# Optimization experiments

Hardware: AMD Instinct MI355X
Metric: run time of the kernel (lower is better)

## Reference

```python
import jax, jax.numpy as jnp
import numpy as np

B, M, N, D = 32, 10, 1000, 128
DEMAND_SCALER, SPEED_SCALER, PREF_SCALER = 40.0, 1.0, 1.0


def _pos_encoding(m, d, dtype):
    # standard sinusoidal PE over agent positions 0..m-1
    pos = jnp.arange(m, dtype=dtype)[:, None]
    div = jnp.exp(jnp.arange(0, d, 2, dtype=dtype) * (-jnp.log(jnp.asarray(10000.0, dtype)) / d))
    ang = pos * div  # (m, d/2)
    return jnp.stack([jnp.sin(ang), jnp.cos(ang)], axis=-1).reshape(m, d)  # even=sin, odd=cos


def setup_inputs() -> dict:
    key = jax.random.key(0)
    ks = jax.random.split(key, 14)
    return {
        "locs": jax.random.uniform(ks[0], (B, M + N, 2), jnp.float32),
        "capacity": jax.random.uniform(ks[1], (B, M), jnp.float32),
        "speed": jax.random.uniform(ks[2], (B, M), jnp.float32),
        "demand": jax.random.uniform(ks[3], (B, 1, M + N), jnp.float32),
        "agents_preference": jax.random.uniform(ks[4], (B, M, M + N), jnp.float32),
        "action_mask": jnp.ones((B, M, M + N), dtype=bool),
        "W_depot": jax.random.normal(ks[5], (D, 2), jnp.float32) * 0.1,
        "W_posproj": jax.random.normal(ks[6], (D, D), jnp.float32) * 0.05,
        "alpha": jnp.ones((1,), jnp.float32),
        "W_agents": jax.random.normal(ks[7], (D, 4), jnp.float32) * 0.1,
        "W_depot_agents": jax.random.normal(ks[8], (D, 2 * D), jnp.float32) * 0.05,
        "W_clients": jax.random.normal(ks[9], (D, 5), jnp.float32) * 0.1,
        "W_pref": jax.random.normal(ks[10], (D, 1), jnp.float32) * 0.1,
        "W_final": jax.random.normal(ks[11], (D, 3 * D), jnp.float32) * 0.05,
    }


def reference(locs, capacity, speed, demand, agents_preference, action_mask,
              W_depot, W_posproj, alpha, W_agents, W_depot_agents, W_clients,
              W_pref, W_final):
    m = action_mask.shape[-2]
    d = W_final.shape[0]
    depot_locs = locs[:, :m]            # (B, m, 2)
    agents_locs = locs[:, :m]
    clients_locs = locs[:, m:]          # (B, N, 2)

    # depot branch with positional encoding
    dep_emb = depot_locs @ W_depot.T                                   # (B, m, D)
    pe = _pos_encoding(m, d, dep_emb.dtype)                            # (m, D)
    depot_embedding = dep_emb + alpha[0] * (pe @ W_posproj.T)          # broadcast over B

    # agents branch
    agents_feats = jnp.concatenate(
        [agents_locs, capacity[..., None] / DEMAND_SCALER, speed[..., None] / SPEED_SCALER], axis=-1)
    agents_embedding = agents_feats @ W_agents.T                       # (B, m, D)
    depot_agents_embedding = jnp.concatenate(
        [depot_embedding, agents_embedding], axis=-1) @ W_depot_agents.T  # (B, m, D)

    # clients branch (with polar feats)
    demands = demand[:, 0, m:]                                         # (B, N)
    centered = clients_locs - depot_locs[:, 0:1]                       # (B, N, 2)
    dist = jnp.linalg.norm(centered, axis=-1, keepdims=True)
    angle = jnp.arctan2(centered[..., 1:], centered[..., :1])
    clients_feats = jnp.concatenate(
        [clients_locs, demands[..., None] / DEMAND_SCALER, dist, angle], axis=-1)
    clients_embedding = clients_feats @ W_clients.T                    # (B, N, D)

    nodes_embedding = jnp.concatenate([agents_embedding, clients_embedding], axis=1)  # (B, m+N, D)

    # fused final projection: Linear(3D, D) on cat([nodes, pref_embed, depot_agents])
    # == nodes @ Wn.T  +  pref_embed @ Wp.T  +  depot_agents @ Wd.T, broadcast over dims.
    # pref_embed = pref[..., None] * W_pref[:, 0]  (rank-1), so pref_embed @ Wp.T = pref[..., None] * (Wp @ W_pref[:, 0])
    Wn, Wp, Wd = W_final[:, :d], W_final[:, d:2 * d], W_final[:, 2 * d:]
    v_pref = Wp @ W_pref[:, 0]                                         # (D,)
    pref = agents_preference / PREF_SCALER                             # (B, m, m+N)
    combined_embedding = (
        (nodes_embedding @ Wn.T)[:, None, :, :]                        # (B, 1, m+N, D)
        + pref[..., None] * v_pref                                     # (B, m, m+N, D)
        + (depot_agents_embedding @ Wd.T)[:, :, None, :]               # (B, m, 1, D)
    )
    return nodes_embedding, combined_embedding
```

## Files before the change

### kernel.cpp

```cpp
#include <hip/hip_runtime.h>
#include <math.h>

#define BB 32
#define MM 10
#define NNODES 1010
#define DD 128
#define RPB 16
#define NG ((NNODES + RPB - 1) / RPB)

__global__ __launch_bounds__(DD) void k_agents(
    const float* __restrict__ locs,
    const float* __restrict__ capacity,
    const float* __restrict__ speed,
    const float* __restrict__ W_depot,
    const float* __restrict__ W_posproj,
    const float* __restrict__ alpha,
    const float* __restrict__ W_agents,
    const float* __restrict__ W_da,
    const float* __restrict__ W_pref,
    const float* __restrict__ W_final,
    float* __restrict__ out_nodes,
    float* __restrict__ ws_daWd,
    float* __restrict__ ws_vpref)
{
    const int b = blockIdx.x / MM;
    const int m = blockIdx.x % MM;
    const int d = threadIdx.x;

    __shared__ float pe_s[DD];
    __shared__ float dep_s[DD];
    __shared__ float ag_s[DD];
    __shared__ float da_s[DD];

    {
        const int i = d >> 1;
        const float div = expf((float)(2 * i) * (-logf(10000.0f) / (float)DD));
        const float ang = (float)m * div;
        pe_s[d] = (d & 1) ? cosf(ang) : sinf(ang);
    }
    __syncthreads();

    float pp = 0.0f;
    {
        const float4* wp = (const float4*)(W_posproj + (size_t)d * DD);
        #pragma unroll 4
        for (int k4 = 0; k4 < DD / 4; ++k4) {
            float4 w = wp[k4];
            const float* p = &pe_s[k4 * 4];
            pp = fmaf(w.x, p[0], pp);
            pp = fmaf(w.y, p[1], pp);
            pp = fmaf(w.z, p[2], pp);
            pp = fmaf(w.w, p[3], pp);
        }
    }

    const float lx = locs[((size_t)b * NNODES + m) * 2 + 0];
    const float ly = locs[((size_t)b * NNODES + m) * 2 + 1];
    const float dep = fmaf(lx, W_depot[d * 2 + 0],
                      fmaf(ly, W_depot[d * 2 + 1], alpha[0] * pp));

    const float cap = capacity[b * MM + m] * (1.0f / 40.0f);
    const float spd = speed[b * MM + m];
    const float ag = fmaf(lx, W_agents[d * 4 + 0],
                     fmaf(ly, W_agents[d * 4 + 1],
                     fmaf(cap, W_agents[d * 4 + 2],
                          spd * W_agents[d * 4 + 3])));

    out_nodes[((size_t)b * NNODES + m) * DD + d] = ag;

    dep_s[d] = dep;
    ag_s[d] = ag;
    __syncthreads();

    float da = 0.0f;
    {
        const float4* wda = (const float4*)(W_da + (size_t)d * 2 * DD);
        #pragma unroll 4
        for (int k4 = 0; k4 < DD / 4; ++k4) {
            float4 w = wda[k4];
            const float* p = &dep_s[k4 * 4];
            da = fmaf(w.x, p[0], da);
            da = fmaf(w.y, p[1], da);
            da = fmaf(w.z, p[2], da);
            da = fmaf(w.w, p[3], da);
        }
        #pragma unroll 4
        for (int k4 = 0; k4 < DD / 4; ++k4) {
            float4 w = wda[DD / 4 + k4];
            const float* p = &ag_s[k4 * 4];
            da = fmaf(w.x, p[0], da);
            da = fmaf(w.y, p[1], da);
            da = fmaf(w.z, p[2], da);
            da = fmaf(w.w, p[3], da);
        }
    }
    da_s[d] = da;
    __syncthreads();

    float dw = 0.0f;
    {
        const float4* wfd = (const float4*)(W_final + (size_t)d * 3 * DD + 2 * DD);
        #pragma unroll 4
        for (int k4 = 0; k4 < DD / 4; ++k4) {
            float4 w = wfd[k4];
            const float* p = &da_s[k4 * 4];
            dw = fmaf(w.x, p[0], dw);
            dw = fmaf(w.y, p[1], dw);
            dw = fmaf(w.z, p[2], dw);
            dw = fmaf(w.w, p[3], dw);
        }
    }
    ws_daWd[(b * MM + m) * DD + d] = dw;

    if (blockIdx.x == 0) {
        float vp = 0.0f;
        const float4* wfp = (const float4*)(W_final + (size_t)d * 3 * DD + DD);
        const float4* prf = (const float4*)W_pref;
        #pragma unroll 4
        for (int k4 = 0; k4 < DD / 4; ++k4) {
            float4 w = wfp[k4];
            float4 p = prf[k4];
            vp = fmaf(w.x, p.x, vp);
            vp = fmaf(w.y, p.y, vp);
            vp = fmaf(w.z, p.z, vp);
            vp = fmaf(w.w, p.w, vp);
        }
        ws_vpref[d] = vp;
    }
}

__global__ __launch_bounds__(DD) void k_main(
    const float* __restrict__ locs,
    const float* __restrict__ demand,
    const float* __restrict__ pref,
    const float* __restrict__ W_clients,
    const float* __restrict__ W_final,
    const float* __restrict__ ws_daWd,
    const float* __restrict__ ws_vpref,
    float* __restrict__ out_nodes,
    float* __restrict__ out_comb)
{
    const int g = blockIdx.x;
    const int b = blockIdx.y;
    const int tid = threadIdx.x;
    const int n0 = g * RPB;

    __shared__ float rows[RPB][DD];
    __shared__ float feat[RPB][5];

    if (tid < RPB) {
        const int node = n0 + tid;
        if (node < NNODES && node >= MM) {
            const float cx = locs[((size_t)b * NNODES + node) * 2 + 0];
            const float cy = locs[((size_t)b * NNODES + node) * 2 + 1];
            const float d0x = locs[((size_t)b * NNODES + 0) * 2 + 0];
            const float d0y = locs[((size_t)b * NNODES + 0) * 2 + 1];
            const float dx = cx - d0x;
            const float dy = cy - d0y;
            feat[tid][0] = cx;
            feat[tid][1] = cy;
            feat[tid][2] = demand[(size_t)b * NNODES + node] * (1.0f / 40.0f);
            feat[tid][3] = sqrtf(fmaf(dx, dx, dy * dy));
            feat[tid][4] = atan2f(dy, dx);
        }
    }
    __syncthreads();

    {
        const float wc0 = W_clients[tid * 5 + 0];
        const float wc1 = W_clients[tid * 5 + 1];
        const float wc2 = W_clients[tid * 5 + 2];
        const float wc3 = W_clients[tid * 5 + 3];
        const float wc4 = W_clients[tid * 5 + 4];
        #pragma unroll
        for (int r = 0; r < RPB; ++r) {
            const int node = n0 + r;
            float val = 0.0f;
            if (node < NNODES) {
                if (node < MM) {
                    val = out_nodes[((size_t)b * NNODES + node) * DD + tid];
                } else {
                    val = fmaf(feat[r][0], wc0,
                          fmaf(feat[r][1], wc1,
                          fmaf(feat[r][2], wc2,
                          fmaf(feat[r][3], wc3,
                               feat[r][4] * wc4))));
                    out_nodes[((size_t)b * NNODES + node) * DD + tid] = val;
                }
            }
            rows[r][tid] = val;
        }
    }
    __syncthreads();

    const int d = tid;
    float acc[RPB];
    #pragma unroll
    for (int r = 0; r < RPB; ++r) acc[r] = 0.0f;

    {
        const float4* wn = (const float4*)(W_final + (size_t)d * 3 * DD);
        #pragma unroll 4
        for (int k4 = 0; k4 < DD / 4; ++k4) {
            const float4 w = wn[k4];
            #pragma unroll
            for (int r = 0; r < RPB; ++r) {
                const float4 p = *(const float4*)&rows[r][k4 * 4];
                acc[r] = fmaf(w.x, p.x,
                         fmaf(w.y, p.y,
                         fmaf(w.z, p.z,
                         fmaf(w.w, p.w, acc[r]))));
            }
        }
    }

    const float vp = ws_vpref[d];
    float dawd[MM];
    #pragma unroll
    for (int mm = 0; mm < MM; ++mm)
        dawd[mm] = ws_daWd[(b * MM + mm) * DD + d];

    for (int r = 0; r < RPB; ++r) {
        const int node = n0 + r;
        if (node >= NNODES) break;
        #pragma unroll
        for (int mm = 0; mm < MM; ++mm) {
            const float pr = pref[(size_t)(b * MM + mm) * NNODES + node];
            out_comb[((size_t)(b * MM + mm) * NNODES + node) * DD + d] =
                fmaf(pr, vp, acc[r] + dawd[mm]);
        }
    }
}

extern "C" void kernel_launch(void* const* d_in, const int* in_sizes, int n_in,
                              void* d_out, int out_size, void* d_ws, size_t ws_size,
                              hipStream_t stream) {
    const float* locs       = (const float*)d_in[0];
    const float* capacity   = (const float*)d_in[1];
    const float* speed      = (const float*)d_in[2];
    const float* demand     = (const float*)d_in[3];
    const float* agents_pref= (const float*)d_in[4];
    const float* W_depot    = (const float*)d_in[6];
    const float* W_posproj  = (const float*)d_in[7];
    const float* alpha      = (const float*)d_in[8];
    const float* W_agents   = (const float*)d_in[9];
    const float* W_da       = (const float*)d_in[10];
    const float* W_clients  = (const float*)d_in[11];
    const float* W_pref     = (const float*)d_in[12];
    const float* W_final    = (const float*)d_in[13];

    float* out_nodes = (float*)d_out;
    float* out_comb  = out_nodes + (size_t)BB * NNODES * DD;

    float* ws_daWd  = (float*)d_ws;
    float* ws_vpref = ws_daWd + BB * MM * DD;

    k_agents<<<dim3(BB * MM), DD, 0, stream>>>(
        locs, capacity, speed, W_depot, W_posproj, alpha, W_agents,
        W_da, W_pref, W_final, out_nodes, ws_daWd, ws_vpref);

    k_main<<<dim3(NG, BB), DD, 0, stream>>>(
        locs, demand, agents_pref, W_clients, W_final,
        ws_daWd, ws_vpref, out_nodes, out_comb);
}
```

Baseline: 256.8 us.

## Retile main kernel to 4x4 register blocks with float4 stores and split-K agents

The main kernel now handles 32 rows per block with 256 threads. Each thread computes a 4-row by 4-column register tile, which gives weight reuse across rows, and writes the combined output with float4 stores. Preference values are staged in shared memory instead of being read as scattered scalars. The agents kernel uses 512 threads and splits each dot product into four K-partials reduced through shared memory, shortening its serial chains. The output write is bandwidth-bound (about 165MB), so wider stores may help, but fewer blocks and higher register pressure are risks.

```diff
diff --git a/kernel.cpp b/kernel.cpp
--- a/kernel.cpp
+++ b/kernel.cpp
@@ -5,10 +5,10 @@
 #define MM 10
 #define NNODES 1010
 #define DD 128
-#define RPB 16
+#define RPB 32
 #define NG ((NNODES + RPB - 1) / RPB)
 
-__global__ __launch_bounds__(DD) void k_agents(
+__global__ __launch_bounds__(512) void k_agents(
     const float* __restrict__ locs,
     const float* __restrict__ capacity,
     const float* __restrict__ speed,
@@ -25,14 +25,17 @@
 {
     const int b = blockIdx.x / MM;
     const int m = blockIdx.x % MM;
-    const int d = threadIdx.x;
+    const int t = threadIdx.x;
+    const int d = t & (DD - 1);
+    const int q = t >> 7;
 
     __shared__ float pe_s[DD];
     __shared__ float dep_s[DD];
     __shared__ float ag_s[DD];
     __shared__ float da_s[DD];
-
-    {
+    __shared__ float part[4][DD];
+
+    if (q == 0) {
         const int i = d >> 1;
         const float div = expf((float)(2 * i) * (-logf(10000.0f) / (float)DD));
         const float ang = (float)m * div;
@@ -42,94 +45,80 @@
 
     float pp = 0.0f;
     {
-        const float4* wp = (const float4*)(W_posproj + (size_t)d * DD);
-        #pragma unroll 4
-        for (int k4 = 0; k4 < DD / 4; ++k4) {
-            float4 w = wp[k4];
-            const float* p = &pe_s[k4 * 4];
-            pp = fmaf(w.x, p[0], pp);
-            pp = fmaf(w.y, p[1], pp);
-            pp = fmaf(w.z, p[2], pp);
-            pp = fmaf(w.w, p[3], pp);
-        }
-    }
-
-    const float lx = locs[((size_t)b * NNODES + m) * 2 + 0];
-    const float ly = locs[((size_t)b * NNODES + m) * 2 + 1];
-    const float dep = fmaf(lx, W_depot[d * 2 + 0],
-                      fmaf(ly, W_depot[d * 2 + 1], alpha[0] * pp));
-
-    const float cap = capacity[b * MM + m] * (1.0f / 40.0f);
-    const float spd = speed[b * MM + m];
-    const float ag = fmaf(lx, W_agents[d * 4 + 0],
-                     fmaf(ly, W_agents[d * 4 + 1],
-                     fmaf(cap, W_agents[d * 4 + 2],
-                          spd * W_agents[d * 4 + 3])));
-
-    out_nodes[((size_t)b * NNODES + m) * DD + d] = ag;
-
-    dep_s[d] = dep;
-    ag_s[d] = ag;
+        const float4* wp  = (const float4*)(W_posproj + (size_t)d * DD + q * 32);
+        const float4* pe4 = (const float4*)(pe_s + q * 32);
+        #pragma unroll
+        for (int k4 = 0; k4 < 8; ++k4) {
+            const float4 w = wp[k4], p = pe4[k4];
+            pp = fmaf(w.x, p.x, fmaf(w.y, p.y, fmaf(w.z, p.z, fmaf(w.w, p.w, pp))));
+        }
+    }
+    part[q][d] = pp;
+    __syncthreads();
+
+    if (q == 0) {
+        const float ppf = part[0][d] + part[1][d] + part[2][d] + part[3][d];
+        const float lx = locs[((size_t)b * NNODES + m) * 2 + 0];
+        const float ly = locs[((size_t)b * NNODES + m) * 2 + 1];
+        const float dep = fmaf(lx, W_depot[d * 2 + 0],
+                          fmaf(ly, W_depot[d * 2 + 1], alpha[0] * ppf));
+        const float cap = capacity[b * MM + m] * (1.0f / 40.0f);
+        const float spd = speed[b * MM + m];
+        const float ag = fmaf(lx, W_agents[d * 4 + 0],
+                         fmaf(ly, W_agents[d * 4 + 1],
+                         fmaf(cap, W_agents[d * 4 + 2],
+                              spd * W_agents[d * 4 + 3])));
+        out_nodes[((size_t)b * NNODES + m) * DD + d] = ag;
+        dep_s[d] = dep;
+        ag_s[d] = ag;
+    }
     __syncthreads();
 
     float da = 0.0f;
     {
-        const float4* wda = (const float4*)(W_da + (size_t)d * 2 * DD);
-        #pragma unroll 4
-        for (int k4 = 0; k4 < DD / 4; ++k4) {
-            float4 w = wda[k4];
-            const float* p = &dep_s[k4 * 4];
-            da = fmaf(w.x, p[0], da);
-            da = fmaf(w.y, p[1], da);
-            da = fmaf(w.z, p[2], da);
-            da = fmaf(w.w, p[3], da);
-        }
-        #pragma unroll 4
-        for (int k4 = 0; k4 < DD / 4; ++k4) {
-            float4 w = wda[DD / 4 + k4];
-            const float* p = &ag_s[k4 * 4];
-            da = fmaf(w.x, p[0], da);
-            da = fmaf(w.y, p[1], da);
-            da = fmaf(w.z, p[2], da);
-            da = fmaf(w.w, p[3], da);
-        }
-    }
-    da_s[d] = da;
+        const float4* s4  = (const float4*)((q < 2) ? (dep_s + q * 64)
+                                                    : (ag_s + (q - 2) * 64));
+        const float4* wda = (const float4*)(W_da + (size_t)d * 2 * DD + q * 64);
+        #pragma unroll
+        for (int k4 = 0; k4 < 16; ++k4) {
+            const float4 w = wda[k4], p = s4[k4];
+            da = fmaf(w.x, p.x, fmaf(w.y, p.y, fmaf(w.z, p.z, fmaf(w.w, p.w, da))));
+        }
+    }
+    part[q][d] = da;
+    __syncthreads();
+    if (q == 0) da_s[d] = part[0][d] + part[1][d] + part[2][d] + part[3][d];
     __syncthreads();
 
     float dw = 0.0f;
     {
-        const float4* wfd = (const float4*)(W_final + (size_t)d * 3 * DD + 2 * DD);
-        #pragma unroll 4
-        for (int k4 = 0; k4 < DD / 4; ++k4) {
-            float4 w = wfd[k4];
-            const float* p = &da_s[k4 * 4];
-            dw = fmaf(w.x, p[0], dw);
-            dw = fmaf(w.y, p[1], dw);
-            dw = fmaf(w.z, p[2], dw);
-            dw = fmaf(w.w, p[3], dw);
-        }
-    }
-    ws_daWd[(b * MM + m) * DD + d] = dw;
-
-    if (blockIdx.x == 0) {
+        const float4* wfd = (const float4*)(W_final + (size_t)d * 3 * DD + 2 * DD + q * 32);
+        const float4* s4  = (const float4*)(da_s + q * 32);
+        #pragma unroll
+        for (int k4 = 0; k4 < 8; ++k4) {
+            const float4 w = wfd[k4], p = s4[k4];
+            dw = fmaf(w.x, p.x, fmaf(w.y, p.y, fmaf(w.z, p.z, fmaf(w.w, p.w, dw))));
+        }
+    }
+    part[q][d] = dw;
+    __syncthreads();
+    if (q == 0)
+        ws_daWd[(b * MM + m) * DD + d] = part[0][d] + part[1][d] + part[2][d] + part[3][d];
+
+    if (blockIdx.x == 0 && q == 3) {
         float vp = 0.0f;
         const float4* wfp = (const float4*)(W_final + (size_t)d * 3 * DD + DD);
         const float4* prf = (const float4*)W_pref;
-        #pragma unroll 4
+        #pragma unroll
         for (int k4 = 0; k4 < DD / 4; ++k4) {
-            float4 w = wfp[k4];
-            float4 p = prf[k4];
-            vp = fmaf(w.x, p.x, vp);
-            vp = fmaf(w.y, p.y, vp);
-            vp = fmaf(w.z, p.z, vp);
-            vp = fmaf(w.w, p.w, vp);
+            const float4 w = wfp[k4], p = prf[k4];
+            vp = fmaf(w.x, p.x, fmaf(w.y, p.y, fmaf(w.z, p.z, fmaf(w.w, p.w, vp))));
         }
         ws_vpref[d] = vp;
     }
 }
 
-__global__ __launch_bounds__(DD) void k_main(
+__global__ __launch_bounds__(256) void k_main(
     const float* __restrict__ locs,
     const float* __restrict__ demand,
     const float* __restrict__ pref,
@@ -142,14 +131,15 @@
 {
     const int g = blockIdx.x;
     const int b = blockIdx.y;
-    const int tid = threadIdx.x;
+    const int t = threadIdx.x;
     const int n0 = g * RPB;
 
     __shared__ float rows[RPB][DD];
     __shared__ float feat[RPB][5];
-
-    if (tid < RPB) {
-        const int node = n0 + tid;
+    __shared__ float pref_s[MM][RPB];
+
+    if (t < RPB) {
+        const int node = n0 + t;
         if (node < NNODES && node >= MM) {
             const float cx = locs[((size_t)b * NNODES + node) * 2 + 0];
             const float cy = locs[((size_t)b * NNODES + node) * 2 + 1];
@@ -157,77 +147,102 @@
             const float d0y = locs[((size_t)b * NNODES + 0) * 2 + 1];
             const float dx = cx - d0x;
             const float dy = cy - d0y;
-            feat[tid][0] = cx;
-            feat[tid][1] = cy;
-            feat[tid][2] = demand[(size_t)b * NNODES + node] * (1.0f / 40.0f);
-            feat[tid][3] = sqrtf(fmaf(dx, dx, dy * dy));
-            feat[tid][4] = atan2f(dy, dx);
-        }
-    }
-    __syncthreads();
-
-    {
-        const float wc0 = W_clients[tid * 5 + 0];
-        const float wc1 = W_clients[tid * 5 + 1];
-        const float wc2 = W_clients[tid * 5 + 2];
-        const float wc3 = W_clients[tid * 5 + 3];
-        const float wc4 = W_clients[tid * 5 + 4];
-        #pragma unroll
-        for (int r = 0; r < RPB; ++r) {
+            feat[t][0] = cx;
+            feat[t][1] = cy;
+            feat[t][2] = demand[(size_t)b * NNODES + node] * (1.0f / 40.0f);
+            feat[t][3] = sqrtf(fmaf(dx, dx, dy * dy));
+            feat[t][4] = atan2f(dy, dx);
+        }
+    }
+    for (int idx = t; idx < MM * RPB; idx += 256) {
+        const int mm = idx >> 5;
+        const int rr = idx & 31;
+        const int node = n0 + rr;
+        pref_s[mm][rr] = (node < NNODES)
+            ? pref[(size_t)(b * MM + mm) * NNODES + node] : 0.0f;
+    }
+    __syncthreads();
+
+    {
+        const int d = t & (DD - 1);
+        const int h = t >> 7;
+        const float wc0 = W_clients[d * 5 + 0];
+        const float wc1 = W_clients[d * 5 + 1];
+        const float wc2 = W_clients[d * 5 + 2];
+        const float wc3 = W_clients[d * 5 + 3];
+        const float wc4 = W_clients[d * 5 + 4];
+        #pragma unroll
+        for (int i = 0; i < RPB / 2; ++i) {
+            const int r = h * (RPB / 2) + i;
             const int node = n0 + r;
             float val = 0.0f;
             if (node < NNODES) {
                 if (node < MM) {
-                    val = out_nodes[((size_t)b * NNODES + node) * DD + tid];
+                    val = out_nodes[((size_t)b * NNODES + node) * DD + d];
                 } else {
                     val = fmaf(feat[r][0], wc0,
                           fmaf(feat[r][1], wc1,
                           fmaf(feat[r][2], wc2,
                           fmaf(feat[r][3], wc3,
                                feat[r][4] * wc4))));
-                    out_nodes[((size_t)b * NNODES + node) * DD + tid] = val;
+                    out_nodes[((size_t)b * NNODES + node) * DD + d] = val;
                 }
             }
-            rows[r][tid] = val;
-        }
-    }
-    __syncthreads();
-
-    const int d = tid;
-    float acc[RPB];
+            rows[r][d] = val;
+        }
+    }
+    __syncthreads();
+
+    const int c = t & 31;
+    const int s = t >> 5;
+    const int col = c * 4;
+    float4 acc[4];
     #pragma unroll
-    for (int r = 0; r < RPB; ++r) acc[r] = 0.0f;
-
-    {
-        const float4* wn = (const float4*)(W_final + (size_t)d * 3 * DD);
+    for (int j = 0; j < 4; ++j) acc[j] = make_float4(0.f, 0.f, 0.f, 0.f);
+
+    {
+        const float* w_base = W_final + (size_t)col * 3 * DD;
         #pragma unroll 4
         for (int k4 = 0; k4 < DD / 4; ++k4) {
-            const float4 w = wn[k4];
+            float4 w[4];
             #pragma unroll
-            for (int r = 0; r < RPB; ++r) {
-                const float4 p = *(const float4*)&rows[r][k4 * 4];
-                acc[r] = fmaf(w.x, p.x,
-                         fmaf(w.y, p.y,
-                         fmaf(w.z, p.z,
-                         fmaf(w.w, p.w, acc[r]))));
+            for (int i = 0; i < 4; ++i)
+                w[i] = *(const float4*)(w_base + (size_t)i * 3 * DD + k4 * 4);
+            #pragma unroll
+            for (int j = 0; j < 4; ++j) {
+                const float4 x = *(const float4*)&rows[s * 4 + j][k4 * 4];
+                acc[j].x = fmaf(x.x, w[0].x, fmaf(x.y, w[0].y,
+                           fmaf(x.z, w[0].z, fmaf(x.w, w[0].w, acc[j].x))));
+                acc[j].y = fmaf(x.x, w[1].x, fmaf(x.y, w[1].y,
+                           fmaf(x.z, w[1].z, fmaf(x.w, w[1].w, acc[j].y))));
+                acc[j].z = fmaf(x.x, w[2].x, fmaf(x.y, w[2].y,
+                           fmaf(x.z, w[2].z, fmaf(x.w, w[2].w, acc[j].z))));
+                acc[j].w = fmaf(x.x, w[3].x, fmaf(x.y, w[3].y,
+                           fmaf(x.z, w[3].z, fmaf(x.w, w[3].w, acc[j].w))));
             }
         }
     }
 
-    const float vp = ws_vpref[d];
-    float dawd[MM];
+    const float4 vp = *(const float4*)(ws_vpref + col);
+    float4 dawd[MM];
     #pragma unroll
     for (int mm = 0; mm < MM; ++mm)
-        dawd[mm] = ws_daWd[(b * MM + mm) * DD + d];
-
-    for (int r = 0; r < RPB; ++r) {
-        const int node = n0 + r;
-        if (node >= NNODES) break;
-        #pragma unroll
-        for (int mm = 0; mm < MM; ++mm) {
-            const float pr = pref[(size_t)(b * MM + mm) * NNODES + node];
-            out_comb[((size_t)(b * MM + mm) * NNODES + node) * DD + d] =
-                fmaf(pr, vp, acc[r] + dawd[mm]);
+        dawd[mm] = *(const float4*)(ws_daWd + (size_t)(b * MM + mm) * DD + col);
+
+    #pragma unroll
+    for (int mm = 0; mm < MM; ++mm) {
+        #pragma unroll
+        for (int j = 0; j < 4; ++j) {
+            const int node = n0 + s * 4 + j;
+            if (node >= NNODES) continue;
+            const float pr = pref_s[mm][s * 4 + j];
+            float4 o;
+            o.x = fmaf(pr, vp.x, acc[j].x + dawd[mm].x);
+            o.y = fmaf(pr, vp.y, acc[j].y + dawd[mm].y);
+            o.z = fmaf(pr, vp.z, acc[j].z + dawd[mm].z);
+            o.w = fmaf(pr, vp.w, acc[j].w + dawd[mm].w);
+            *(float4*)(out_comb +
+                ((size_t)(b * MM + mm) * NNODES + node) * DD + col) = o;
         }
     }
 }
@@ -235,19 +250,19 @@
 extern "C" void kernel_launch(void* const* d_in, const int* in_sizes, int n_in,
                               void* d_out, int out_size, void* d_ws, size_t ws_size,
                               hipStream_t stream) {
-    const float* locs       = (const float*)d_in[0];
-    const float* capacity   = (const float*)d_in[1];
-    const float* speed      = (const float*)d_in[2];
-    const float* demand     = (const float*)d_in[3];
-    const float* agents_pref= (const float*)d_in[4];
-    const float* W_depot    = (const float*)d_in[6];
-    const float* W_posproj  = (const float*)d_in[7];
-    const float* alpha      = (const float*)d_in[8];
-    const float* W_agents   = (const float*)d_in[9];
-    const float* W_da       = (const float*)d_in[10];
-    const float* W_clients  = (const float*)d_in[11];
-    const float* W_pref     = (const float*)d_in[12];
-    const float* W_final    = (const float*)d_in[13];
+    const float* locs        = (const float*)d_in[0];
+    const float* capacity    = (const float*)d_in[1];
+    const float* speed       = (const float*)d_in[2];
+    const float* demand      = (const float*)d_in[3];
+    const float* agents_pref = (const float*)d_in[4];
+    const float* W_depot     = (const float*)d_in[6];
+    const float* W_posproj   = (const float*)d_in[7];
+    const float* alpha       = (const float*)d_in[8];
+    const float* W_agents    = (const float*)d_in[9];
+    const float* W_da        = (const float*)d_in[10];
+    const float* W_clients   = (const float*)d_in[11];
+    const float* W_pref      = (const float*)d_in[12];
+    const float* W_final     = (const float*)d_in[13];
 
     float* out_nodes = (float*)d_out;
     float* out_comb  = out_nodes + (size_t)BB * NNODES * DD;
@@ -255,11 +270,11 @@
     float* ws_daWd  = (float*)d_ws;
     float* ws_vpref = ws_daWd + BB * MM * DD;
 
-    k_agents<<<dim3(BB * MM), DD, 0, stream>>>(
+    k_agents<<<dim3(BB * MM), 512, 0, stream>>>(
         locs, capacity, speed, W_depot, W_posproj, alpha, W_agents,
         W_da, W_pref, W_final, out_nodes, ws_daWd, ws_vpref);
 
-    k_main<<<dim3(NG, BB), DD, 0, stream>>>(
+    k_main<<<dim3(NG, BB), 256, 0, stream>>>(
         locs, demand, agents_pref, W_clients, W_final,
         ws_daWd, ws_vpref, out_nodes, out_comb);
 }
```

New measurement: 268.5 us. +4.6%, slower.
